# Kernel tuning notes

Measured on AMD Instinct MI355X. Metric: run time of the kernel, lower is better.

Reference implementation:

```python
import jax, jax.numpy as jnp
import numpy as np

GRAY_THRESHOLD = 127.5  # undefined global in source; midpoint of [0,255] implied by Convert_to_0_255
N_BINS = 512            # 3x3 binary pattern -> codes 0..511
DILATION = 1

# LBP-style fixed conv weights: powers of two laid out row-major
_LBP_W = jnp.array([[256., 128., 64.],
                    [32.,  16.,  8.],
                    [4.,   2.,   1.]], dtype=jnp.float32).reshape(1, 1, 3, 3)  # OIHW


def _pattern_hist(img):
    # img: [N,1,H,W] in [-1,1]-ish range
    x = (img * 0.5 + 0.5) * 255.0          # Convert_to_0_255
    b = (x > GRAY_THRESHOLD).astype(jnp.float32)  # binarize
    # 3x3 valid conv with dilation encodes each 3x3 binary neighborhood as an int code 0..511
    codes = jax.lax.conv_general_dilated(
        b, _LBP_W, window_strides=(1, 1), padding='VALID',
        rhs_dilation=(DILATION, DILATION),
        dimension_numbers=('NCHW', 'OIHW', 'NCHW'))
    idx = codes.reshape(-1).astype(jnp.int32)  # exact integers, int cast == torch .int()
    n = idx.shape[0]
    counts = jnp.zeros((N_BINS,), jnp.float32).at[idx].add(1.0)  # bincount(minlength=512)
    return counts / n


def setup_inputs() -> dict:
    key = jax.random.key(0)
    k1, k2 = jax.random.split(key)
    input = jax.random.normal(k1, (64, 1, 512, 512), dtype=jnp.float32)
    target = jax.random.normal(k2, (64, 1, 512, 512), dtype=jnp.float32)
    return {"input": input, "target": target}


def reference(input, target):
    N, C, H, W = input.shape
    h_in = _pattern_hist(input)
    h_tgt = _pattern_hist(target)
    s = jnp.mean((h_in - h_tgt) ** 2)  # nn.MSELoss
    return s / N / C
```

## Files before the change

### kernel.cpp

```cpp
#include <hip/hip_runtime.h>
#include <stdint.h>

#define HH 512
#define WW 512
#define NIMG 64
#define OH 510
#define OW 510
#define NPB 4096
#define HBINS (NPB + 64)
#define SEGR 16
#define NSEG 32
#define NREP 8
#define BLOCK 1024
#define WPB (BLOCK / 64)
#define NBLK 512
#define NWAVE (NBLK * WPB)
#define NBIG (NIMG * 2 * NSEG * 2)
#define NSEAM (NIMG * 2 * 8)

typedef float f4 __attribute__((ext_vector_type(4)));

__device__ __forceinline__ f4 ldg4(const float* addr) {
    f4 r;
    asm volatile("global_load_dwordx4 %0, %1, off" : "=v"(r) : "v"(addr));
    return r;
}
template<int N>
__device__ __forceinline__ void waitv(f4& x) {
    if      constexpr (N == 7) asm volatile("s_waitcnt vmcnt(7)" : "+v"(x));
    else if constexpr (N == 6) asm volatile("s_waitcnt vmcnt(6)" : "+v"(x));
    else if constexpr (N == 5) asm volatile("s_waitcnt vmcnt(5)" : "+v"(x));
    else if constexpr (N == 4) asm volatile("s_waitcnt vmcnt(4)" : "+v"(x));
    else if constexpr (N == 3) asm volatile("s_waitcnt vmcnt(3)" : "+v"(x));
    else if constexpr (N == 2) asm volatile("s_waitcnt vmcnt(2)" : "+v"(x));
    else if constexpr (N == 1) asm volatile("s_waitcnt vmcnt(1)" : "+v"(x));
    else                       asm volatile("s_waitcnt vmcnt(0)" : "+v"(x));
}

#define BINC 0x1p-24f

__device__ __forceinline__ int pack4(f4 v) {
    return (v.x > BINC) | ((v.y > BINC) << 1) | ((v.z > BINC) << 2) | ((v.w > BINC) << 3);
}

__global__ __launch_bounds__(BLOCK) void hist_kernel(const float* __restrict__ inp,
                                                     const float* __restrict__ tgt,
                                                     int* __restrict__ rep) {
    __shared__ int hist[HBINS];
    const int tid  = threadIdx.x;
    const int lane = tid & 63;
    const int wave = tid >> 6;

    for (int i = tid; i < HBINS; i += BLOCK) hist[i] = 0;
    __syncthreads();

    const int wid   = blockIdx.x * WPB + wave;
    const int dummy = NPB + ((lane + wave * 8) & 63);
    const bool ln_ok = (lane < 63);

    {
        const int task = wid;
        const int tile = task & 1;
        const int seg  = (task >> 1) & 31;
        const int t    = (task >> 6) & 1;
        const int img  = task >> 7;
        const int r0   = seg * SEGR;
        const int R    = min(SEGR, OH - r0);
        const int c0   = tile * 256 + 4 * lane;
        const int sign = 1 - 2 * t;
        const float* base = (t ? tgt : inp) + (size_t)img * (HH * WW) + c0;
        auto ap = [&](int rel) { return base + (size_t)min(r0 + rel, HH - 1) * WW; };

        f4 X[8];
        #pragma unroll
        for (int q = 0; q < 8; ++q) X[q] = ldg4(ap(q));

        int n0, n1, n2;
        waitv<7>(X[0]);
        { int nib = pack4(X[0]); n0 = nib | (__shfl_down(nib, 1) << 4); }
        X[0] = ldg4(ap(8));
        waitv<7>(X[1]);
        { int nib = pack4(X[1]); n1 = nib | (__shfl_down(nib, 1) << 4); }
        X[1] = ldg4(ap(9));

        #define STEP(o, W) { \
            f4& Xs = X[((o) + 2) & 7]; \
            waitv<W>(Xs); \
            int nib = pack4(Xs); \
            n2 = nib | (__shfl_down(nib, 1) << 4); \
            if ((o) <= 7) Xs = ldg4(ap((o) + 10)); \
            if ((o) < R) { \
                int p01 = (n0 & 15) | ((n1 & 15) << 4) | ((n2 & 15) << 8); \
                int p23 = ((n0 >> 2) & 15) | (((n1 >> 2) & 15) << 4) \
                        | (((n2 >> 2) & 15) << 8); \
                atomicAdd(&hist[p01], sign); \
                atomicAdd(&hist[ln_ok ? p23 : dummy], sign); \
            } \
            n0 = n1; n1 = n2; }

        STEP(0, 7)  STEP(1, 7)  STEP(2, 7)  STEP(3, 7)
        STEP(4, 7)  STEP(5, 7)  STEP(6, 7)  STEP(7, 7)
        STEP(8, 7)  STEP(9, 6)  STEP(10, 5) STEP(11, 4)
        STEP(12, 3) STEP(13, 2) STEP(14, 1) STEP(15, 0)
        #undef STEP
    }

    if ((wid & 7) == 0) {
        const int idx = wid >> 3;
        const int seg = idx & 7;
        const int t   = (idx >> 3) & 1;
        const int img = idx >> 4;
        const int sign = 1 - 2 * t;
        const int r   = seg * 64 + lane;
        const bool v  = (r < OH);
        const float* bp = (t ? tgt : inp) + (size_t)img * (HH * WW);
        int p[3];
        #pragma unroll
        for (int q = 0; q < 3; ++q) {
            const float* rowp = bp + (size_t)min(r + q, HH - 1) * WW;
            float2 A = *(const float2*)(rowp + 254);
            float2 B = *(const float2*)(rowp + 256);
            p[q] = (A.x > BINC) | ((A.y > BINC) << 1)
                 | ((B.x > BINC) << 2) | ((B.y > BINC) << 3);
        }
        int pair = p[0] | (p[1] << 4) | (p[2] << 8);
        atomicAdd(&hist[v ? pair : dummy], sign);
    }

    __syncthreads();
    const int rid = blockIdx.x & (NREP - 1);
    for (int i = tid; i < NPB; i += BLOCK) {
        int vv = hist[i];
        if (vv) atomicAdd(&rep[rid * NPB + i], vv);
    }
}

__global__ __launch_bounds__(1024) void reduce_kernel(const int* __restrict__ rep,
                                                      float* __restrict__ out) {
    __shared__ int sh[512];
    __shared__ double sd[512];
    const int tid = threadIdx.x;
    if (tid < 512) sh[tid] = 0;
    __syncthreads();

    #pragma unroll
    for (int k = 0; k < NPB / 1024; ++k) {
        int p = tid + k * 1024;
        int s = 0;
        #pragma unroll
        for (int r = 0; r < NREP; ++r) s += rep[r * NPB + p];
        if (s) {
            int f0 = (p & 7) | (((p >> 4) & 7) << 3) | (((p >> 8) & 7) << 6);
            int f1 = ((p >> 1) & 7) | (((p >> 5) & 7) << 3) | (((p >> 9) & 7) << 6);
            atomicAdd(&sh[f0], s);
            atomicAdd(&sh[f1], s);
        }
    }
    __syncthreads();

    if (tid < 512) { double d = (double)sh[tid]; sd[tid] = d * d; }
    __syncthreads();
    for (int stp = 256; stp > 0; stp >>= 1) {
        if (tid < stp) sd[tid] += sd[tid + stp];
        __syncthreads();
    }
    if (tid == 0) {
        const double n = (double)NIMG * OH * OW;
        out[0] = (float)(sd[0] / (n * n) / 512.0 / 64.0);
    }
}

extern "C" void kernel_launch(void* const* d_in, const int* in_sizes, int n_in,
                              void* d_out, int out_size, void* d_ws, size_t ws_size,
                              hipStream_t stream) {
    const float* inp = (const float*)d_in[0];
    const float* tgt = (const float*)d_in[1];
    float* out = (float*)d_out;
    int* rep = (int*)d_ws;

    hipMemsetAsync(rep, 0, NREP * NPB * sizeof(int), stream);
    hist_kernel<<<NBLK, BLOCK, 0, stream>>>(inp, tgt, rep);
    reduce_kernel<<<1, 1024, 0, stream>>>(rep, out);
}
```

Before: 149.9 us.

## Fuse final reduction into histogram kernel via last-block ticket and double rows per wave

The separate reduce kernel launch is removed. Each block bumps an atomic ticket after flushing its histogram, and the last block to arrive performs the fold-to-512-bins and MSE reduction. Each wave now processes 32 output rows instead of 16, which halves the block count and the number of replica buffers, so fewer blocks flush their 4096-bin histograms to global memory. The cost is less parallelism: 256 blocks of 1024 threads on a 256-CU part, with a longer serial load chain per wave. The last block also runs the reduction as a tail after all other blocks finish.

```diff
diff --git a/kernel.cpp b/kernel.cpp
--- a/kernel.cpp
+++ b/kernel.cpp
@@ -8,15 +8,15 @@
 #define OW 510
 #define NPB 4096
 #define HBINS (NPB + 64)
-#define SEGR 16
-#define NSEG 32
-#define NREP 8
+#define SEGR 32
+#define NSEG 16
+#define NREP 4
 #define BLOCK 1024
 #define WPB (BLOCK / 64)
-#define NBLK 512
+#define NBLK 256
 #define NWAVE (NBLK * WPB)
 #define NBIG (NIMG * 2 * NSEG * 2)
-#define NSEAM (NIMG * 2 * 8)
+#define TICKET (NREP * NPB)
 
 typedef float f4 __attribute__((ext_vector_type(4)));
 
@@ -45,8 +45,12 @@
 
 __global__ __launch_bounds__(BLOCK) void hist_kernel(const float* __restrict__ inp,
                                                      const float* __restrict__ tgt,
-                                                     int* __restrict__ rep) {
+                                                     int* __restrict__ rep,
+                                                     float* __restrict__ out) {
     __shared__ int hist[HBINS];
+    __shared__ int sh[512];
+    __shared__ double sd[512];
+    __shared__ int lastflag;
     const int tid  = threadIdx.x;
     const int lane = tid & 63;
     const int wave = tid >> 6;
@@ -61,9 +65,9 @@
     {
         const int task = wid;
         const int tile = task & 1;
-        const int seg  = (task >> 1) & 31;
-        const int t    = (task >> 6) & 1;
-        const int img  = task >> 7;
+        const int seg  = (task >> 1) & (NSEG - 1);
+        const int t    = (task >> 5) & 1;
+        const int img  = task >> 6;
         const int r0   = seg * SEGR;
         const int R    = min(SEGR, OH - r0);
         const int c0   = tile * 256 + 4 * lane;
@@ -88,7 +92,7 @@
             waitv<W>(Xs); \
             int nib = pack4(Xs); \
             n2 = nib | (__shfl_down(nib, 1) << 4); \
-            if ((o) <= 7) Xs = ldg4(ap((o) + 10)); \
+            if ((o) <= 23) Xs = ldg4(ap((o) + 10)); \
             if ((o) < R) { \
                 int p01 = (n0 & 15) | ((n1 & 15) << 4) | ((n2 & 15) << 8); \
                 int p23 = ((n0 >> 2) & 15) | (((n1 >> 2) & 15) << 4) \
@@ -100,13 +104,17 @@
 
         STEP(0, 7)  STEP(1, 7)  STEP(2, 7)  STEP(3, 7)
         STEP(4, 7)  STEP(5, 7)  STEP(6, 7)  STEP(7, 7)
-        STEP(8, 7)  STEP(9, 6)  STEP(10, 5) STEP(11, 4)
-        STEP(12, 3) STEP(13, 2) STEP(14, 1) STEP(15, 0)
+        STEP(8, 7)  STEP(9, 7)  STEP(10, 7) STEP(11, 7)
+        STEP(12, 7) STEP(13, 7) STEP(14, 7) STEP(15, 7)
+        STEP(16, 7) STEP(17, 7) STEP(18, 7) STEP(19, 7)
+        STEP(20, 7) STEP(21, 7) STEP(22, 7) STEP(23, 7)
+        STEP(24, 7) STEP(25, 6) STEP(26, 5) STEP(27, 4)
+        STEP(28, 3) STEP(29, 2) STEP(30, 1) STEP(31, 0)
         #undef STEP
     }
 
-    if ((wid & 7) == 0) {
-        const int idx = wid >> 3;
+    if ((wid & 3) == 0) {
+        const int idx = wid >> 2;
         const int seg = idx & 7;
         const int t   = (idx >> 3) & 1;
         const int img = idx >> 4;
@@ -133,22 +141,26 @@
         int vv = hist[i];
         if (vv) atomicAdd(&rep[rid * NPB + i], vv);
     }
-}
 
-__global__ __launch_bounds__(1024) void reduce_kernel(const int* __restrict__ rep,
-                                                      float* __restrict__ out) {
-    __shared__ int sh[512];
-    __shared__ double sd[512];
-    const int tid = threadIdx.x;
+    __threadfence();
+    if (tid == 0) {
+        int prev = __hip_atomic_fetch_add(&rep[TICKET], 1, __ATOMIC_ACQ_REL,
+                                          __HIP_MEMORY_SCOPE_AGENT);
+        lastflag = (prev == NBLK - 1);
+    }
+    __syncthreads();
+    if (!lastflag) return;
+
     if (tid < 512) sh[tid] = 0;
     __syncthreads();
-
     #pragma unroll
-    for (int k = 0; k < NPB / 1024; ++k) {
-        int p = tid + k * 1024;
+    for (int k = 0; k < NPB / BLOCK; ++k) {
+        int p = tid + k * BLOCK;
         int s = 0;
         #pragma unroll
-        for (int r = 0; r < NREP; ++r) s += rep[r * NPB + p];
+        for (int r = 0; r < NREP; ++r)
+            s += __hip_atomic_load(&rep[r * NPB + p], __ATOMIC_RELAXED,
+                                   __HIP_MEMORY_SCOPE_AGENT);
         if (s) {
             int f0 = (p & 7) | (((p >> 4) & 7) << 3) | (((p >> 8) & 7) << 6);
             int f1 = ((p >> 1) & 7) | (((p >> 5) & 7) << 3) | (((p >> 9) & 7) << 6);
@@ -178,7 +190,6 @@
     float* out = (float*)d_out;
     int* rep = (int*)d_ws;
 
-    hipMemsetAsync(rep, 0, NREP * NPB * sizeof(int), stream);
-    hist_kernel<<<NBLK, BLOCK, 0, stream>>>(inp, tgt, rep);
-    reduce_kernel<<<1, 1024, 0, stream>>>(rep, out);
+    hipMemsetAsync(rep, 0, (NREP * NPB + 1) * sizeof(int), stream);
+    hist_kernel<<<NBLK, BLOCK, 0, stream>>>(inp, tgt, rep, out);
 }
```

New measurement: 212.4 us. 1.42x slower.
